# Kernel tuning notes

Measured on AMD Instinct MI355X. Metric: run time of the kernel, lower is better.

Reference implementation:

```python
import jax, jax.numpy as jnp
import numpy as np

NUM_NODES = 4000
SEQ_LEN = 96
LATENT_DIM = 32
GCN_LAYERS = 2
B = 4
NT = NUM_NODES + SEQ_LEN  # 4096


def setup_inputs() -> dict:
    key = jax.random.key(0)
    k_x, k_w = jax.random.split(key)
    X = jax.random.normal(k_x, (B, NT, LATENT_DIM), dtype=jnp.float32) * 0.1
    # per-layer weights for the graph conv (HeteroFASTGCN-style message passing)
    W = jax.random.normal(k_w, (GCN_LAYERS, LATENT_DIM, LATENT_DIM), dtype=jnp.float32) * (1.0 / np.sqrt(LATENT_DIM))
    return {"X": X, "W": W}


def reference(X, W):
    # STGraphConstructor: node_embs = concat(spatial, temporal) == X
    # adj = tanh(relu(X X^T) + I); dense equivalent of the per-batch nonzero
    # edge extraction (sparse edges carry exactly the nonzero adj entries,
    # so weighted scatter-aggregation == adj @ H).
    sim = jnp.einsum('bnf,bmf->bnm', X, X)          # (B, NT, NT)
    eye = jnp.eye(NT, dtype=X.dtype)
    adj = jnp.tanh(jax.nn.relu(sim) + eye)
    # graph conv: gcn_layers of weighted aggregation + linear + elu
    H = X
    for l in range(GCN_LAYERS):
        H = jax.nn.elu(jnp.einsum('bnm,bmf,fg->bng', adj, H, W[l]))
    # GraphEmbeeding is identity on H
    return H
```

## Files before the change

### kernel.cpp

```cpp
#include <hip/hip_runtime.h>

#define NTOT 4096
#define FD 32
#define BATCH 4

typedef __attribute__((ext_vector_type(8))) _Float16 half8;
typedef __attribute__((ext_vector_type(4))) _Float16 half4;
typedef __attribute__((ext_vector_type(2))) _Float16 half2v;
typedef __attribute__((ext_vector_type(4))) float f32x4;

__device__ __forceinline__ float tanh_pos(float t) {
    float u = __builtin_amdgcn_exp2f(t * 2.885390081777927f);
    float r = __builtin_amdgcn_rcpf(u + 1.0f);
    return __builtin_fmaf(-2.0f, r, 1.0f);
}

__device__ __forceinline__ float tanh_poly_f32(float t) {
    float t2 = t * t;
    float c = __builtin_fmaf(t2, 0.1333333333f, -0.3333333333f);
    return __builtin_fmaf(t * t2, c, t);
}

__device__ __forceinline__ float eluf(float x) {
    return x > 0.0f ? x : (__builtin_amdgcn_exp2f(x * 1.4426950408889634f) - 1.0f);
}

__device__ __forceinline__ half4 pack_relu_poly(f32x4 s) {
    half2v a = __builtin_bit_cast(half2v, __builtin_amdgcn_cvt_pkrtz(s[0], s[1]));
    half2v b = __builtin_bit_cast(half2v, __builtin_amdgcn_cvt_pkrtz(s[2], s[3]));
    const half2v zero = {(_Float16)0.0f, (_Float16)0.0f};
    const half2v mth = {(_Float16)(-0.33333334f), (_Float16)(-0.33333334f)};
    const half2v one = {(_Float16)1.0f, (_Float16)1.0f};
    a = __builtin_elementwise_max(a, zero);
    b = __builtin_elementwise_max(b, zero);
    half2v a2 = a * a, b2 = b * b;
    half2v ca = a2 * mth + one, cb = b2 * mth + one;
    a = a * ca;
    b = b * cb;
    return __builtin_shufflevector(a, b, 0, 1, 2, 3);
}

__device__ __forceinline__ half4 diag_transform(f32x4 s, int l15, int lg) {
    float t[4];
#pragma unroll
    for (int e = 0; e < 4; ++e) t[e] = fmaxf(s[e], 0.0f);
#pragma unroll
    for (int e = 0; e < 4; ++e) {
        bool d = (lg * 4 + e == l15);
        t[e] = d ? tanh_pos(t[e] + 1.0f) : tanh_poly_f32(t[e]);
    }
    return __builtin_shufflevector(
        __builtin_bit_cast(half2v, __builtin_amdgcn_cvt_pkrtz(t[0], t[1])),
        __builtin_bit_cast(half2v, __builtin_amdgcn_cvt_pkrtz(t[2], t[3])), 0, 1, 2, 3);
}

__global__ __launch_bounds__(256) void convert_x(const float* __restrict__ X,
                                                 _Float16* __restrict__ Kfrag,
                                                 _Float16* __restrict__ Vfrag) {
    __shared__ float lds[128 * 33];
    const int tid = threadIdx.x;
    const int blk = blockIdx.x;
    const int xcd = blk & 7;
    const int batch = xcd >> 1;
    const int chunk = ((xcd & 1) << 4) | (blk >> 3);
    const int nbase = chunk << 7;

    const float* Xp = X + ((size_t)batch * NTOT + nbase) * FD;
#pragma unroll
    for (int k = 0; k < 16; ++k) {
        int e = tid + k * 256;
        lds[(e >> 5) * 33 + (e & 31)] = Xp[e];
    }
    __syncthreads();

    {
        _Float16* kout = Kfrag + (size_t)batch * NTOT * FD + (size_t)(nbase >> 4) * 512;
        const int tl = tid >> 5;
        const int l0 = (tid & 31) * 2;
#pragma unroll
        for (int s = 0; s < 2; ++s) {
            int l = l0 + s;
            int row = tl * 16 + (l & 15);
            int cb = (l >> 4) * 8;
            half8 v;
#pragma unroll
            for (int j = 0; j < 8; ++j) v[j] = (_Float16)lds[row * 33 + cb + j];
            *(half8*)(kout + (tl * 64 + l) * 8) = v;
        }
    }
    {
        _Float16* vout = Vfrag + (size_t)batch * NTOT * FD + (size_t)(nbase >> 4) * 512;
        const int tl = tid >> 5;
        const int fh = (tid >> 4) & 1;
        const int lb = (tid & 15) * 4;
#pragma unroll
        for (int li = 0; li < 4; ++li) {
            int lane = lb + li;
            int l15 = lane & 15, lg = lane >> 4;
            half4 v;
#pragma unroll
            for (int j = 0; j < 4; ++j)
                v[j] = (_Float16)lds[(tl * 16 + lg * 4 + j) * 33 + fh * 16 + l15];
            *(half4*)(vout + ((tl * 2 + fh) * 64 + lane) * 4) = v;
        }
    }
}

template <int LAYER>
__global__ __launch_bounds__(1024, 4) void gcn_layer_kernel(const _Float16* __restrict__ Kf,
                                                            const _Float16* __restrict__ Vf,
                                                            const float* __restrict__ Wg,
                                                            _Float16* __restrict__ outHt,
                                                            float* __restrict__ outF) {
    __shared__ _Float16 lds_part[16 * 64 * 32];

    const int tid = threadIdx.x;
    const int lane = tid & 63;
    const int wv = tid >> 6;
    const int blk = blockIdx.x;
    const int xcd = blk & 7;
    const int b = xcd >> 1;
    const int rowidx = ((xcd & 1) << 5) | (blk >> 3);
    const int rowbase = rowidx << 6;
    const int l15 = lane & 15;
    const int lg = lane >> 4;

    const _Float16* KfB = Kf + (size_t)b * NTOT * FD;
    const _Float16* VfB = Vf + (size_t)b * NTOT * FD;

    half8 q[4];
#pragma unroll
    for (int qt = 0; qt < 4; ++qt)
        q[qt] = *(const half8*)(KfB + (size_t)((rowbase >> 4) + qt) * 512 + lane * 8);

    const int col0 = wv << 8;
    const _Float16* kq = KfB + (size_t)(col0 >> 4) * 512 + lane * 8;
    const _Float16* vq = VfB + (size_t)(col0 >> 4) * 512 + lane * 4;

    f32x4 accA[4], accB[4];
#pragma unroll
    for (int qt = 0; qt < 4; ++qt) {
        accA[qt] = (f32x4){0.f, 0.f, 0.f, 0.f};
        accB[qt] = (f32x4){0.f, 0.f, 0.f, 0.f};
    }
    const f32x4 zero = {0.f, 0.f, 0.f, 0.f};

    const int diagA = (rowbase - col0) >> 5;

#pragma unroll
    for (int it = 0; it < 8; ++it) {
        const int base = it * 1024;
        half8 k0 = *(const half8*)(kq + base);
        half8 k1 = *(const half8*)(kq + base + 512);
        half4 v00 = *(const half4*)(vq + base);
        half4 v01 = *(const half4*)(vq + base + 256);
        half4 v10 = *(const half4*)(vq + base + 512);
        half4 v11 = *(const half4*)(vq + base + 768);

        f32x4 s0[4], s1[4];
#pragma unroll
        for (int qt = 0; qt < 4; ++qt) {
            s0[qt] = __builtin_amdgcn_mfma_f32_16x16x32_f16(k0, q[qt], zero, 0, 0, 0);
            s1[qt] = __builtin_amdgcn_mfma_f32_16x16x32_f16(k1, q[qt], zero, 0, 0, 0);
        }

        half4 p0[4], p1[4];
#pragma unroll
        for (int qt = 0; qt < 4; ++qt) {
            p0[qt] = pack_relu_poly(s0[qt]);
            p1[qt] = pack_relu_poly(s1[qt]);
        }
        if (it == diagA) {
            p0[0] = diag_transform(s0[0], l15, lg);
            p1[1] = diag_transform(s1[1], l15, lg);
        }
        if (it == diagA + 1) {
            p0[2] = diag_transform(s0[2], l15, lg);
            p1[3] = diag_transform(s1[3], l15, lg);
        }

#pragma unroll
        for (int qt = 0; qt < 4; ++qt) {
            accA[qt] = __builtin_amdgcn_mfma_f32_16x16x16f16(v00, p0[qt], accA[qt], 0, 0, 0);
            accB[qt] = __builtin_amdgcn_mfma_f32_16x16x16f16(v01, p0[qt], accB[qt], 0, 0, 0);
            accA[qt] = __builtin_amdgcn_mfma_f32_16x16x16f16(v10, p1[qt], accA[qt], 0, 0, 0);
            accB[qt] = __builtin_amdgcn_mfma_f32_16x16x16f16(v11, p1[qt], accB[qt], 0, 0, 0);
        }
    }

#pragma unroll
    for (int qt = 0; qt < 4; ++qt) {
        half4 pa = __builtin_shufflevector(
            __builtin_bit_cast(half2v, __builtin_amdgcn_cvt_pkrtz(accA[qt][0], accA[qt][1])),
            __builtin_bit_cast(half2v, __builtin_amdgcn_cvt_pkrtz(accA[qt][2], accA[qt][3])), 0, 1, 2, 3);
        half4 pb = __builtin_shufflevector(
            __builtin_bit_cast(half2v, __builtin_amdgcn_cvt_pkrtz(accB[qt][0], accB[qt][1])),
            __builtin_bit_cast(half2v, __builtin_amdgcn_cvt_pkrtz(accB[qt][2], accB[qt][3])), 0, 1, 2, 3);
        int r = qt * 16 + l15;
        *(half4*)(lds_part + (wv * 64 + r) * 32 + lg * 4) = pa;
        *(half4*)(lds_part + (wv * 64 + r) * 32 + 16 + lg * 4) = pb;
    }
    __syncthreads();

    float red0 = 0.0f, red1 = 0.0f;
#pragma unroll
    for (int ww = 0; ww < 16; ++ww) {
        red0 += (float)lds_part[ww * 2048 + tid];
        red1 += (float)lds_part[ww * 2048 + tid + 1024];
    }
    __syncthreads();
    float* ldsf = (float*)lds_part;
    ldsf[tid] = red0;
    ldsf[tid + 1024] = red1;
    __syncthreads();

    if (LAYER == 0) {
        const int jp = tid & 1;
        const int lane_v = (tid >> 1) & 63;
        const int fh = (tid >> 7) & 1;
        const int tl = tid >> 8;
        const int g = fh * 16 + (lane_v & 15);
        const int r0 = tl * 16 + ((lane_v >> 4) << 2) + jp * 2;
        float a0 = 0.0f, a1 = 0.0f;
#pragma unroll
        for (int f = 0; f < FD; ++f) {
            float w = Wg[f * FD + g];
            a0 = __builtin_fmaf(ldsf[r0 * FD + f], w, a0);
            a1 = __builtin_fmaf(ldsf[(r0 + 1) * FD + f], w, a1);
        }
        a0 = eluf(a0);
        a1 = eluf(a1);
        unsigned pk = __builtin_bit_cast(unsigned, __builtin_amdgcn_cvt_pkrtz(a0, a1));
        _Float16* dst = outHt + (size_t)b * NTOT * FD +
                        ((size_t)(((rowbase >> 4) + tl) * 2 + fh) * 64 + lane_v) * 4 + jp * 2;
        *(unsigned*)dst = pk;
    } else {
        const int g = tid & 31, r0 = tid >> 5;
        float a0 = 0.0f, a1 = 0.0f;
#pragma unroll
        for (int f = 0; f < FD; ++f) {
            float w = Wg[f * FD + g];
            a0 = __builtin_fmaf(ldsf[r0 * FD + f], w, a0);
            a1 = __builtin_fmaf(ldsf[(r0 + 32) * FD + f], w, a1);
        }
        a0 = eluf(a0);
        a1 = eluf(a1);
        float* dst = outF + ((size_t)b * NTOT + rowbase) * FD + g;
        dst[(size_t)r0 * FD] = a0;
        dst[(size_t)(r0 + 32) * FD] = a1;
    }
}

extern "C" void kernel_launch(void* const* d_in, const int* in_sizes, int n_in,
                              void* d_out, int out_size, void* d_ws, size_t ws_size,
                              hipStream_t stream) {
    const float* X = (const float*)d_in[0];
    const float* W = (const float*)d_in[1];
    float* out = (float*)d_out;

    _Float16* Kfrag = (_Float16*)d_ws;
    _Float16* VfragX = Kfrag + (size_t)BATCH * NTOT * FD;
    _Float16* H1frag = VfragX + (size_t)BATCH * NTOT * FD;

    convert_x<<<128, 256, 0, stream>>>(X, Kfrag, VfragX);
    gcn_layer_kernel<0><<<256, 1024, 0, stream>>>(Kfrag, VfragX, W, H1frag, nullptr);
    gcn_layer_kernel<1><<<256, 1024, 0, stream>>>(Kfrag, H1frag, W + FD * FD, nullptr, out);
}
```

Measured before the change: 37.34 us.

## Stream K/V fragments through double-buffered LDS via async global_load_lds

```diff
diff --git a/kernel.cpp b/kernel.cpp
--- a/kernel.cpp
+++ b/kernel.cpp
@@ -54,6 +54,11 @@
         __builtin_bit_cast(half2v, __builtin_amdgcn_cvt_pkrtz(t[2], t[3])), 0, 1, 2, 3);
 }
 
+__device__ __forceinline__ void gll16(const void* g, void* l) {
+    __builtin_amdgcn_global_load_lds((const __attribute__((address_space(1))) void*)g,
+                                     (__attribute__((address_space(3))) void*)l, 16, 0, 0);
+}
+
 __global__ __launch_bounds__(256) void convert_x(const float* __restrict__ X,
                                                  _Float16* __restrict__ Kfrag,
                                                  _Float16* __restrict__ Vfrag) {
@@ -112,7 +117,7 @@
                                                             const float* __restrict__ Wg,
                                                             _Float16* __restrict__ outHt,
                                                             float* __restrict__ outF) {
-    __shared__ _Float16 lds_part[16 * 64 * 32];
+    __shared__ _Float16 smem[65536];
 
     const int tid = threadIdx.x;
     const int lane = tid & 63;
@@ -134,8 +139,9 @@
         q[qt] = *(const half8*)(KfB + (size_t)((rowbase >> 4) + qt) * 512 + lane * 8);
 
     const int col0 = wv << 8;
-    const _Float16* kq = KfB + (size_t)(col0 >> 4) * 512 + lane * 8;
-    const _Float16* vq = VfB + (size_t)(col0 >> 4) * 512 + lane * 4;
+    const _Float16* kg = KfB + (size_t)(col0 >> 4) * 512 + lane * 8;
+    const _Float16* vg = VfB + (size_t)(col0 >> 4) * 512 + lane * 8;
+    _Float16* wbase = smem + wv * 4096;
 
     f32x4 accA[4], accB[4];
 #pragma unroll
@@ -148,14 +154,26 @@
     const int diagA = (rowbase - col0) >> 5;
 
 #pragma unroll
+    for (int it = 0; it < 2; ++it) {
+        _Float16* lb = wbase + (it & 1) * 2048;
+        gll16(kg + it * 1024, lb);
+        gll16(kg + it * 1024 + 512, lb + 512);
+        gll16(vg + it * 1024, lb + 1024);
+        gll16(vg + it * 1024 + 512, lb + 1536);
+    }
+
+#pragma unroll
     for (int it = 0; it < 8; ++it) {
-        const int base = it * 1024;
-        half8 k0 = *(const half8*)(kq + base);
-        half8 k1 = *(const half8*)(kq + base + 512);
-        half4 v00 = *(const half4*)(vq + base);
-        half4 v01 = *(const half4*)(vq + base + 256);
-        half4 v10 = *(const half4*)(vq + base + 512);
-        half4 v11 = *(const half4*)(vq + base + 768);
+        if (it < 7) asm volatile("s_waitcnt vmcnt(4)" ::: "memory");
+        else        asm volatile("s_waitcnt vmcnt(0)" ::: "memory");
+
+        const _Float16* rb = wbase + (it & 1) * 2048;
+        half8 k0 = *(const half8*)(rb + lane * 8);
+        half8 k1 = *(const half8*)(rb + 512 + lane * 8);
+        half4 v00 = *(const half4*)(rb + 1024 + lane * 4);
+        half4 v01 = *(const half4*)(rb + 1280 + lane * 4);
+        half4 v10 = *(const half4*)(rb + 1536 + lane * 4);
+        half4 v11 = *(const half4*)(rb + 1792 + lane * 4);
 
         f32x4 s0[4], s1[4];
 #pragma unroll
@@ -186,8 +204,19 @@
             accA[qt] = __builtin_amdgcn_mfma_f32_16x16x16f16(v10, p1[qt], accA[qt], 0, 0, 0);
             accB[qt] = __builtin_amdgcn_mfma_f32_16x16x16f16(v11, p1[qt], accB[qt], 0, 0, 0);
         }
-    }
-
+
+        if (it < 6) {
+            _Float16* lb = wbase + (it & 1) * 2048;
+            gll16(kg + (it + 2) * 1024, lb);
+            gll16(kg + (it + 2) * 1024 + 512, lb + 512);
+            gll16(vg + (it + 2) * 1024, lb + 1024);
+            gll16(vg + (it + 2) * 1024 + 512, lb + 1536);
+        }
+    }
+
+    __syncthreads();
+
+    _Float16* lds_part = smem;
 #pragma unroll
     for (int qt = 0; qt < 4; ++qt) {
         half4 pa = __builtin_shufflevector(
@@ -209,7 +238,7 @@
         red1 += (float)lds_part[ww * 2048 + tid + 1024];
     }
     __syncthreads();
-    float* ldsf = (float*)lds_part;
+    float* ldsf = (float*)smem;
     ldsf[tid] = red0;
     ldsf[tid + 1024] = red1;
     __syncthreads();
```

New measurement: 42.24 us. +13.1%, slower.

## Fuse conversion and both GCN layers into one persistent kernel with grid barriers

Applied to the files above, without the earlier changes.

```diff
diff --git a/kernel.cpp b/kernel.cpp
--- a/kernel.cpp
+++ b/kernel.cpp
@@ -3,6 +3,7 @@
 #define NTOT 4096
 #define FD 32
 #define BATCH 4
+#define NBLK 256
 
 typedef __attribute__((ext_vector_type(8))) _Float16 half8;
 typedef __attribute__((ext_vector_type(4))) _Float16 half4;
@@ -54,65 +55,26 @@
         __builtin_bit_cast(half2v, __builtin_amdgcn_cvt_pkrtz(t[2], t[3])), 0, 1, 2, 3);
 }
 
-__global__ __launch_bounds__(256) void convert_x(const float* __restrict__ X,
-                                                 _Float16* __restrict__ Kfrag,
-                                                 _Float16* __restrict__ Vfrag) {
-    __shared__ float lds[128 * 33];
-    const int tid = threadIdx.x;
-    const int blk = blockIdx.x;
-    const int xcd = blk & 7;
-    const int batch = xcd >> 1;
-    const int chunk = ((xcd & 1) << 4) | (blk >> 3);
-    const int nbase = chunk << 7;
-
-    const float* Xp = X + ((size_t)batch * NTOT + nbase) * FD;
-#pragma unroll
-    for (int k = 0; k < 16; ++k) {
-        int e = tid + k * 256;
-        lds[(e >> 5) * 33 + (e & 31)] = Xp[e];
-    }
+__device__ __forceinline__ void grid_barrier(unsigned* ctr) {
     __syncthreads();
-
-    {
-        _Float16* kout = Kfrag + (size_t)batch * NTOT * FD + (size_t)(nbase >> 4) * 512;
-        const int tl = tid >> 5;
-        const int l0 = (tid & 31) * 2;
-#pragma unroll
-        for (int s = 0; s < 2; ++s) {
-            int l = l0 + s;
-            int row = tl * 16 + (l & 15);
-            int cb = (l >> 4) * 8;
-            half8 v;
-#pragma unroll
-            for (int j = 0; j < 8; ++j) v[j] = (_Float16)lds[row * 33 + cb + j];
-            *(half8*)(kout + (tl * 64 + l) * 8) = v;
-        }
-    }
-    {
-        _Float16* vout = Vfrag + (size_t)batch * NTOT * FD + (size_t)(nbase >> 4) * 512;
-        const int tl = tid >> 5;
-        const int fh = (tid >> 4) & 1;
-        const int lb = (tid & 15) * 4;
-#pragma unroll
-        for (int li = 0; li < 4; ++li) {
-            int lane = lb + li;
-            int l15 = lane & 15, lg = lane >> 4;
-            half4 v;
-#pragma unroll
-            for (int j = 0; j < 4; ++j)
-                v[j] = (_Float16)lds[(tl * 16 + lg * 4 + j) * 33 + fh * 16 + l15];
-            *(half4*)(vout + ((tl * 2 + fh) * 64 + lane) * 4) = v;
-        }
-    }
-}
-
-template <int LAYER>
-__global__ __launch_bounds__(1024, 4) void gcn_layer_kernel(const _Float16* __restrict__ Kf,
-                                                            const _Float16* __restrict__ Vf,
-                                                            const float* __restrict__ Wg,
-                                                            _Float16* __restrict__ outHt,
-                                                            float* __restrict__ outF) {
-    __shared__ _Float16 lds_part[16 * 64 * 32];
+    if (threadIdx.x == 0) {
+        __builtin_amdgcn_fence(__ATOMIC_RELEASE, "agent");
+        __hip_atomic_fetch_add(ctr, 1u, __ATOMIC_RELAXED, __HIP_MEMORY_SCOPE_AGENT);
+        while (__hip_atomic_load(ctr, __ATOMIC_RELAXED, __HIP_MEMORY_SCOPE_AGENT) < (unsigned)NBLK)
+            __builtin_amdgcn_s_sleep(2);
+        __builtin_amdgcn_fence(__ATOMIC_ACQUIRE, "agent");
+    }
+    __syncthreads();
+}
+
+__global__ __launch_bounds__(1024, 4) void fused_gcn(const float* __restrict__ X,
+                                                     const float* __restrict__ Wg,
+                                                     float* __restrict__ outF,
+                                                     _Float16* __restrict__ Kf,
+                                                     _Float16* __restrict__ Vf,
+                                                     _Float16* __restrict__ H1,
+                                                     unsigned* __restrict__ bar) {
+    __shared__ char smem_raw[65536];
 
     const int tid = threadIdx.x;
     const int lane = tid & 63;
@@ -125,8 +87,46 @@
     const int l15 = lane & 15;
     const int lg = lane >> 4;
 
-    const _Float16* KfB = Kf + (size_t)b * NTOT * FD;
-    const _Float16* VfB = Vf + (size_t)b * NTOT * FD;
+    _Float16* KfB = Kf + (size_t)b * NTOT * FD;
+    _Float16* VfB = Vf + (size_t)b * NTOT * FD;
+    _Float16* H1B = H1 + (size_t)b * NTOT * FD;
+
+    {
+        float* clds = (float*)smem_raw;
+        const float* Xp = X + ((size_t)b * NTOT + rowbase) * FD;
+#pragma unroll
+        for (int k = 0; k < 2; ++k) {
+            int e = tid * 2 + k;
+            clds[(e >> 5) * 33 + (e & 31)] = Xp[e];
+        }
+        __syncthreads();
+
+        {
+            const int tl = tid >> 8;
+            const int l = (tid >> 2) & 63;
+            const int jj = (tid & 3) * 2;
+            const int row = tl * 16 + (l & 15);
+            const int cb = (l >> 4) * 8 + jj;
+            _Float16 h0 = (_Float16)clds[row * 33 + cb];
+            _Float16 h1 = (_Float16)clds[row * 33 + cb + 1];
+            half2v pk = {h0, h1};
+            _Float16* dst = KfB + (size_t)((rowbase >> 4) + tl) * 512 + l * 8 + jj;
+            *(unsigned*)dst = __builtin_bit_cast(unsigned, pk);
+        }
+        {
+            const int tl = tid >> 8;
+            const int fh = (tid >> 7) & 1;
+            const int lv = (tid >> 1) & 63;
+            const int jp = (tid & 1) * 2;
+            const int vl15 = lv & 15, vlg = lv >> 4;
+            _Float16 h0 = (_Float16)clds[(tl * 16 + vlg * 4 + jp) * 33 + fh * 16 + vl15];
+            _Float16 h1 = (_Float16)clds[(tl * 16 + vlg * 4 + jp + 1) * 33 + fh * 16 + vl15];
+            half2v pk = {h0, h1};
+            _Float16* dst = VfB + (size_t)(((rowbase >> 4) + tl) * 2 + fh) * 256 + lv * 4 + jp;
+            *(unsigned*)dst = __builtin_bit_cast(unsigned, pk);
+        }
+    }
+    grid_barrier(bar);
 
     half8 q[4];
 #pragma unroll
@@ -134,120 +134,128 @@
         q[qt] = *(const half8*)(KfB + (size_t)((rowbase >> 4) + qt) * 512 + lane * 8);
 
     const int col0 = wv << 8;
-    const _Float16* kq = KfB + (size_t)(col0 >> 4) * 512 + lane * 8;
-    const _Float16* vq = VfB + (size_t)(col0 >> 4) * 512 + lane * 4;
-
-    f32x4 accA[4], accB[4];
-#pragma unroll
-    for (int qt = 0; qt < 4; ++qt) {
-        accA[qt] = (f32x4){0.f, 0.f, 0.f, 0.f};
-        accB[qt] = (f32x4){0.f, 0.f, 0.f, 0.f};
-    }
+    const int diagA = (rowbase - col0) >> 5;
     const f32x4 zero = {0.f, 0.f, 0.f, 0.f};
-
-    const int diagA = (rowbase - col0) >> 5;
-
-#pragma unroll
-    for (int it = 0; it < 8; ++it) {
-        const int base = it * 1024;
-        half8 k0 = *(const half8*)(kq + base);
-        half8 k1 = *(const half8*)(kq + base + 512);
-        half4 v00 = *(const half4*)(vq + base);
-        half4 v01 = *(const half4*)(vq + base + 256);
-        half4 v10 = *(const half4*)(vq + base + 512);
-        half4 v11 = *(const half4*)(vq + base + 768);
-
-        f32x4 s0[4], s1[4];
+    _Float16* lds_part = (_Float16*)smem_raw;
+    float* ldsf = (float*)smem_raw;
+
+#pragma unroll 1
+    for (int layer = 0; layer < 2; ++layer) {
+        const _Float16* Vsrc = (layer == 0) ? VfB : H1B;
+        const float* W = Wg + layer * FD * FD;
+        const _Float16* kq = KfB + (size_t)(col0 >> 4) * 512 + lane * 8;
+        const _Float16* vq = Vsrc + (size_t)(col0 >> 4) * 512 + lane * 4;
+
+        f32x4 accA[4], accB[4];
 #pragma unroll
         for (int qt = 0; qt < 4; ++qt) {
-            s0[qt] = __builtin_amdgcn_mfma_f32_16x16x32_f16(k0, q[qt], zero, 0, 0, 0);
-            s1[qt] = __builtin_amdgcn_mfma_f32_16x16x32_f16(k1, q[qt], zero, 0, 0, 0);
-        }
-
-        half4 p0[4], p1[4];
+            accA[qt] = zero;
+            accB[qt] = zero;
+        }
+
+#pragma unroll
+        for (int it = 0; it < 8; ++it) {
+            const int base = it * 1024;
+            half8 k0 = *(const half8*)(kq + base);
+            half8 k1 = *(const half8*)(kq + base + 512);
+            half4 v00 = *(const half4*)(vq + base);
+            half4 v01 = *(const half4*)(vq + base + 256);
+            half4 v10 = *(const half4*)(vq + base + 512);
+            half4 v11 = *(const half4*)(vq + base + 768);
+
+            f32x4 s0[4], s1[4];
+#pragma unroll
+            for (int qt = 0; qt < 4; ++qt) {
+                s0[qt] = __builtin_amdgcn_mfma_f32_16x16x32_f16(k0, q[qt], zero, 0, 0, 0);
+                s1[qt] = __builtin_amdgcn_mfma_f32_16x16x32_f16(k1, q[qt], zero, 0, 0, 0);
+            }
+
+            half4 p0[4], p1[4];
+#pragma unroll
+            for (int qt = 0; qt < 4; ++qt) {
+                p0[qt] = pack_relu_poly(s0[qt]);
+                p1[qt] = pack_relu_poly(s1[qt]);
+            }
+            if (it == diagA) {
+                p0[0] = diag_transform(s0[0], l15, lg);
+                p1[1] = diag_transform(s1[1], l15, lg);
+            }
+            if (it == diagA + 1) {
+                p0[2] = diag_transform(s0[2], l15, lg);
+                p1[3] = diag_transform(s1[3], l15, lg);
+            }
+
+#pragma unroll
+            for (int qt = 0; qt < 4; ++qt) {
+                accA[qt] = __builtin_amdgcn_mfma_f32_16x16x16f16(v00, p0[qt], accA[qt], 0, 0, 0);
+                accB[qt] = __builtin_amdgcn_mfma_f32_16x16x16f16(v01, p0[qt], accB[qt], 0, 0, 0);
+                accA[qt] = __builtin_amdgcn_mfma_f32_16x16x16f16(v10, p1[qt], accA[qt], 0, 0, 0);
+                accB[qt] = __builtin_amdgcn_mfma_f32_16x16x16f16(v11, p1[qt], accB[qt], 0, 0, 0);
+            }
+        }
+
+        __syncthreads();
 #pragma unroll
         for (int qt = 0; qt < 4; ++qt) {
-            p0[qt] = pack_relu_poly(s0[qt]);
-            p1[qt] = pack_relu_poly(s1[qt]);
-        }
-        if (it == diagA) {
-            p0[0] = diag_transform(s0[0], l15, lg);
-            p1[1] = diag_transform(s1[1], l15, lg);
-        }
-        if (it == diagA + 1) {
-            p0[2] = diag_transform(s0[2], l15, lg);
-            p1[3] = diag_transform(s1[3], l15, lg);
-        }
-
-#pragma unroll
-        for (int qt = 0; qt < 4; ++qt) {
-            accA[qt] = __builtin_amdgcn_mfma_f32_16x16x16f16(v00, p0[qt], accA[qt], 0, 0, 0);
-            accB[qt] = __builtin_amdgcn_mfma_f32_16x16x16f16(v01, p0[qt], accB[qt], 0, 0, 0);
-            accA[qt] = __builtin_amdgcn_mfma_f32_16x16x16f16(v10, p1[qt], accA[qt], 0, 0, 0);
-            accB[qt] = __builtin_amdgcn_mfma_f32_16x16x16f16(v11, p1[qt], accB[qt], 0, 0, 0);
-        }
-    }
-
-#pragma unroll
-    for (int qt = 0; qt < 4; ++qt) {
-        half4 pa = __builtin_shufflevector(
-            __builtin_bit_cast(half2v, __builtin_amdgcn_cvt_pkrtz(accA[qt][0], accA[qt][1])),
-            __builtin_bit_cast(half2v, __builtin_amdgcn_cvt_pkrtz(accA[qt][2], accA[qt][3])), 0, 1, 2, 3);
-        half4 pb = __builtin_shufflevector(
-            __builtin_bit_cast(half2v, __builtin_amdgcn_cvt_pkrtz(accB[qt][0], accB[qt][1])),
-            __builtin_bit_cast(half2v, __builtin_amdgcn_cvt_pkrtz(accB[qt][2], accB[qt][3])), 0, 1, 2, 3);
-        int r = qt * 16 + l15;
-        *(half4*)(lds_part + (wv * 64 + r) * 32 + lg * 4) = pa;
-        *(half4*)(lds_part + (wv * 64 + r) * 32 + 16 + lg * 4) = pb;
-    }
-    __syncthreads();
-
-    float red0 = 0.0f, red1 = 0.0f;
-#pragma unroll
-    for (int ww = 0; ww < 16; ++ww) {
-        red0 += (float)lds_part[ww * 2048 + tid];
-        red1 += (float)lds_part[ww * 2048 + tid + 1024];
-    }
-    __syncthreads();
-    float* ldsf = (float*)lds_part;
-    ldsf[tid] = red0;
-    ldsf[tid + 1024] = red1;
-    __syncthreads();
-
-    if (LAYER == 0) {
-        const int jp = tid & 1;
-        const int lane_v = (tid >> 1) & 63;
-        const int fh = (tid >> 7) & 1;
-        const int tl = tid >> 8;
-        const int g = fh * 16 + (lane_v & 15);
-        const int r0 = tl * 16 + ((lane_v >> 4) << 2) + jp * 2;
-        float a0 = 0.0f, a1 = 0.0f;
-#pragma unroll
-        for (int f = 0; f < FD; ++f) {
-            float w = Wg[f * FD + g];
-            a0 = __builtin_fmaf(ldsf[r0 * FD + f], w, a0);
-            a1 = __builtin_fmaf(ldsf[(r0 + 1) * FD + f], w, a1);
-        }
-        a0 = eluf(a0);
-        a1 = eluf(a1);
-        unsigned pk = __builtin_bit_cast(unsigned, __builtin_amdgcn_cvt_pkrtz(a0, a1));
-        _Float16* dst = outHt + (size_t)b * NTOT * FD +
-                        ((size_t)(((rowbase >> 4) + tl) * 2 + fh) * 64 + lane_v) * 4 + jp * 2;
-        *(unsigned*)dst = pk;
-    } else {
-        const int g = tid & 31, r0 = tid >> 5;
-        float a0 = 0.0f, a1 = 0.0f;
-#pragma unroll
-        for (int f = 0; f < FD; ++f) {
-            float w = Wg[f * FD + g];
-            a0 = __builtin_fmaf(ldsf[r0 * FD + f], w, a0);
-            a1 = __builtin_fmaf(ldsf[(r0 + 32) * FD + f], w, a1);
-        }
-        a0 = eluf(a0);
-        a1 = eluf(a1);
-        float* dst = outF + ((size_t)b * NTOT + rowbase) * FD + g;
-        dst[(size_t)r0 * FD] = a0;
-        dst[(size_t)(r0 + 32) * FD] = a1;
+            half4 pa = __builtin_shufflevector(
+                __builtin_bit_cast(half2v, __builtin_amdgcn_cvt_pkrtz(accA[qt][0], accA[qt][1])),
+                __builtin_bit_cast(half2v, __builtin_amdgcn_cvt_pkrtz(accA[qt][2], accA[qt][3])), 0, 1, 2, 3);
+            half4 pb = __builtin_shufflevector(
+                __builtin_bit_cast(half2v, __builtin_amdgcn_cvt_pkrtz(accB[qt][0], accB[qt][1])),
+                __builtin_bit_cast(half2v, __builtin_amdgcn_cvt_pkrtz(accB[qt][2], accB[qt][3])), 0, 1, 2, 3);
+            int r = qt * 16 + l15;
+            *(half4*)(lds_part + (wv * 64 + r) * 32 + lg * 4) = pa;
+            *(half4*)(lds_part + (wv * 64 + r) * 32 + 16 + lg * 4) = pb;
+        }
+        __syncthreads();
+
+        float red0 = 0.0f, red1 = 0.0f;
+#pragma unroll
+        for (int ww = 0; ww < 16; ++ww) {
+            red0 += (float)lds_part[ww * 2048 + tid];
+            red1 += (float)lds_part[ww * 2048 + tid + 1024];
+        }
+        __syncthreads();
+        ldsf[tid] = red0;
+        ldsf[tid + 1024] = red1;
+        __syncthreads();
+
+        if (layer == 0) {
+            const int jp = tid & 1;
+            const int lane_v = (tid >> 1) & 63;
+            const int fh = (tid >> 7) & 1;
+            const int tl = tid >> 8;
+            const int g = fh * 16 + (lane_v & 15);
+            const int r0 = tl * 16 + ((lane_v >> 4) << 2) + jp * 2;
+            float a0 = 0.0f, a1 = 0.0f;
+#pragma unroll
+            for (int f = 0; f < FD; ++f) {
+                float w = W[f * FD + g];
+                a0 = __builtin_fmaf(ldsf[r0 * FD + f], w, a0);
+                a1 = __builtin_fmaf(ldsf[(r0 + 1) * FD + f], w, a1);
+            }
+            a0 = eluf(a0);
+            a1 = eluf(a1);
+            unsigned pk = __builtin_bit_cast(unsigned, __builtin_amdgcn_cvt_pkrtz(a0, a1));
+            _Float16* dst = H1B +
+                ((size_t)(((rowbase >> 4) + tl) * 2 + fh) * 64 + lane_v) * 4 + jp * 2;
+            *(unsigned*)dst = pk;
+            grid_barrier(bar + 16);
+        } else {
+            const int g = tid & 31, r0 = tid >> 5;
+            float a0 = 0.0f, a1 = 0.0f;
+#pragma unroll
+            for (int f = 0; f < FD; ++f) {
+                float w = W[f * FD + g];
+                a0 = __builtin_fmaf(ldsf[r0 * FD + f], w, a0);
+                a1 = __builtin_fmaf(ldsf[(r0 + 32) * FD + f], w, a1);
+            }
+            a0 = eluf(a0);
+            a1 = eluf(a1);
+            float* dst = outF + ((size_t)b * NTOT + rowbase) * FD + g;
+            dst[(size_t)r0 * FD] = a0;
+            dst[(size_t)(r0 + 32) * FD] = a1;
+        }
     }
 }
 
@@ -261,8 +269,8 @@
     _Float16* Kfrag = (_Float16*)d_ws;
     _Float16* VfragX = Kfrag + (size_t)BATCH * NTOT * FD;
     _Float16* H1frag = VfragX + (size_t)BATCH * NTOT * FD;
-
-    convert_x<<<128, 256, 0, stream>>>(X, Kfrag, VfragX);
-    gcn_layer_kernel<0><<<256, 1024, 0, stream>>>(Kfrag, VfragX, W, H1frag, nullptr);
-    gcn_layer_kernel<1><<<256, 1024, 0, stream>>>(Kfrag, H1frag, W + FD * FD, nullptr, out);
-}
+    unsigned* bar = (unsigned*)((char*)d_ws + 3u * 1024 * 1024);
+
+    (void)hipMemsetAsync(bar, 0, 128, stream);
+    fused_gcn<<<NBLK, 1024, 0, stream>>>(X, W, out, Kfrag, VfragX, H1frag, bar);
+}
```

Result: slower. 79.30 us (+112.3%).
